# Performance work log

Hardware: AMD Instinct MI355X
Metric: run time of the kernel (lower is better)

Reference implementation:

```python
import jax, jax.numpy as jnp
import numpy as np

N, F, H = 4096, 256, 4

def setup_inputs() -> dict:
    key = jax.random.key(0)
    kx, kw, kb = jax.random.split(key, 3)
    x = jax.random.normal(kx, (N, F), dtype=jnp.float32)
    # per-head Linear(2F -> 1): weight [H, 2F], bias [H]
    lim = 1.0 / np.sqrt(2 * F)
    W = jax.random.uniform(kw, (H, 2 * F), minval=-lim, maxval=lim, dtype=jnp.float32)
    b = jax.random.uniform(kb, (H,), minval=-lim, maxval=lim, dtype=jnp.float32)
    return {"x": x, "W": W, "b": b}

def reference(x, W, b):
    n, f = x.shape
    # concat(x_i, x_j) @ w^T == x_i @ w1 + x_j @ w2  (separable score, same math)
    W1, W2 = W[:, :f], W[:, f:]            # [H,F] each
    s_i = x @ W1.T                          # [N,H] contribution of row node i
    s_j = x @ W2.T                          # [N,H] contribution of col node j
    # logits[h,i,j] = s_i[i,h] + s_j[j,h] + b[h]
    logits = s_i.T[:, :, None] + s_j.T[:, None, :] + b[:, None, None]  # [H,N,N]
    attn = jax.nn.softmax(logits, axis=2)   # softmax over neighbors j
    out_heads = jnp.einsum('hij,jf->hif', attn, x)  # [H,N,F]
    avg = jnp.mean(out_heads, axis=0)       # [N,F]
    return jax.nn.leaky_relu(avg, negative_slope=0.2)
```

## Files before the change

### kernel.cpp

```cpp
#include <hip/hip_runtime.h>


#define NROWS 4096
#define FDIM  256
#define HHEADS 4
#define RPB 64
#define NB1 (NROWS / RPB)
#define PAD 260


__global__ __launch_bounds__(256) void k1_partials(const float* __restrict__ x,
                                                   const float* __restrict__ W,
                                                   float* __restrict__ partU,
                                                   float* __restrict__ partZ) {
    __shared__ float x_lds[RPB * PAD];
    __shared__ float w_lds[HHEADS * FDIM];
    __shared__ float e_lds[RPB * HHEADS];

    const int t = threadIdx.x;
    const int row0 = blockIdx.x * RPB;

    for (int i = t; i < HHEADS * FDIM; i += 256) {
        int h = i >> 8, c = i & 255;
        w_lds[i] = W[h * (2 * FDIM) + FDIM + c];
    }
    for (int i = t; i < RPB * (FDIM / 4); i += 256) {
        int r = i >> 6, c4 = i & 63;
        float4 v = ((const float4*)x)[(size_t)(row0 + r) * (FDIM / 4) + c4];
        *(float4*)&x_lds[r * PAD + c4 * 4] = v;
    }
    __syncthreads();

    {
        int r = t >> 2, h = t & 3;
        const float4* xr = (const float4*)&x_lds[r * PAD];
        const float4* wr = (const float4*)&w_lds[h * FDIM];
        float acc = 0.f;
        #pragma unroll 8
        for (int c = 0; c < FDIM / 4; ++c) {
            float4 a = xr[c], b = wr[c];
            acc = fmaf(a.x, b.x, fmaf(a.y, b.y, fmaf(a.z, b.z, fmaf(a.w, b.w, acc))));
        }
        e_lds[r * 4 + h] = __expf(acc);
    }
    __syncthreads();

    if (t < HHEADS) {
        float z = 0.f;
        for (int r = 0; r < RPB; ++r) z += e_lds[r * 4 + t];
        partZ[blockIdx.x * HHEADS + t] = z;
    }

    float a0 = 0.f, a1 = 0.f, a2 = 0.f, a3 = 0.f;
    for (int r = 0; r < RPB; ++r) {
        float xv = x_lds[r * PAD + t];
        float4 e4 = *(const float4*)&e_lds[r * 4];
        a0 = fmaf(e4.x, xv, a0);
        a1 = fmaf(e4.y, xv, a1);
        a2 = fmaf(e4.z, xv, a2);
        a3 = fmaf(e4.w, xv, a3);
    }
    float* pu = partU + (size_t)blockIdx.x * (HHEADS * FDIM);
    pu[0 * FDIM + t] = a0;
    pu[1 * FDIM + t] = a1;
    pu[2 * FDIM + t] = a2;
    pu[3 * FDIM + t] = a3;
}

__global__ __launch_bounds__(256) void k2_out(const float* __restrict__ partU,
                                              const float* __restrict__ partZ,
                                              float* __restrict__ out) {
    __shared__ float v_lds[FDIM];
    __shared__ float zinv[HHEADS];
    const int t = threadIdx.x;

    if (t < HHEADS) {
        float z = 0.f;
        for (int b = 0; b < NB1; ++b) z += partZ[b * HHEADS + t];
        zinv[t] = 1.0f / z;
    }

    float u0 = 0.f, u1 = 0.f, u2 = 0.f, u3 = 0.f;
    for (int b = 0; b < NB1; ++b) {
        const float* p = partU + (size_t)b * (HHEADS * FDIM);
        u0 += p[0 * FDIM + t];
        u1 += p[1 * FDIM + t];
        u2 += p[2 * FDIM + t];
        u3 += p[3 * FDIM + t];
    }
    __syncthreads();

    float val = 0.25f * (u0 * zinv[0] + u1 * zinv[1] + u2 * zinv[2] + u3 * zinv[3]);
    v_lds[t] = val > 0.f ? val : 0.2f * val;
    __syncthreads();

    const int row0 = blockIdx.x * 64;
    float4* out4 = (float4*)out;
    #pragma unroll
    for (int i = 0; i < 16; ++i) {
        int idx = t + i * 256;
        int r = idx >> 6, c4 = idx & 63;
        out4[(size_t)(row0 + r) * (FDIM / 4) + c4] = *(const float4*)&v_lds[c4 * 4];
    }
}

extern "C" void kernel_launch(void* const* d_in, const int* in_sizes, int n_in,
                              void* d_out, int out_size, void* d_ws, size_t ws_size,
                              hipStream_t stream) {
    const float* x = (const float*)d_in[0];
    const float* W = (const float*)d_in[1];
    float* partU = (float*)d_ws;
    float* partZ = partU + (size_t)NB1 * HHEADS * FDIM;
    float* out = (float*)d_out;

    k1_partials<<<NB1, 256, 0, stream>>>(x, W, partU, partZ);
    k2_out<<<NROWS / 64, 256, 0, stream>>>(partU, partZ, out);
}
```

Baseline: 74.34 us.

## Split reduction into a separate parallel kernel and widen the partial-sum grid

The first kernel now processes 32 rows per block over 128 blocks, and each row/head dot product is split across two threads and combined with a shuffle. The old output kernel, where every block redundantly summed all partials serially, is replaced by a small reduction kernel spread over 16 blocks that writes the 256-element result vector once. A separate broadcast kernel then fills the output from that vector. This removes redundant reduction work and raises parallelism, at the cost of a third kernel launch.

```diff
diff --git a/kernel.cpp b/kernel.cpp
--- a/kernel.cpp
+++ b/kernel.cpp
@@ -3,10 +3,10 @@
 
 #define NROWS 4096
 #define FDIM  256
-#define HHEADS 4
-#define RPB 64
-#define NB1 (NROWS / RPB)
-#define PAD 260
+#define HH    4
+#define RPB   32
+#define NB1   128
+#define PAD   260
 
 
 __global__ __launch_bounds__(256) void k1_partials(const float* __restrict__ x,
@@ -14,13 +14,13 @@
                                                    float* __restrict__ partU,
                                                    float* __restrict__ partZ) {
     __shared__ float x_lds[RPB * PAD];
-    __shared__ float w_lds[HHEADS * FDIM];
-    __shared__ float e_lds[RPB * HHEADS];
+    __shared__ float w_lds[HH * FDIM];
+    __shared__ float e_lds[RPB * HH];
 
     const int t = threadIdx.x;
     const int row0 = blockIdx.x * RPB;
 
-    for (int i = t; i < HHEADS * FDIM; i += 256) {
+    for (int i = t; i < HH * FDIM; i += 256) {
         int h = i >> 8, c = i & 255;
         w_lds[i] = W[h * (2 * FDIM) + FDIM + c];
     }
@@ -32,23 +32,25 @@
     __syncthreads();
 
     {
-        int r = t >> 2, h = t & 3;
+        int pair = t >> 1, half = t & 1;
+        int r = pair >> 2, h = pair & 3;
         const float4* xr = (const float4*)&x_lds[r * PAD];
         const float4* wr = (const float4*)&w_lds[h * FDIM];
         float acc = 0.f;
-        #pragma unroll 8
-        for (int c = 0; c < FDIM / 4; ++c) {
+        #pragma unroll
+        for (int c = half * 32; c < half * 32 + 32; ++c) {
             float4 a = xr[c], b = wr[c];
             acc = fmaf(a.x, b.x, fmaf(a.y, b.y, fmaf(a.z, b.z, fmaf(a.w, b.w, acc))));
         }
-        e_lds[r * 4 + h] = __expf(acc);
+        acc += __shfl_xor(acc, 1);
+        if (half == 0) e_lds[r * 4 + h] = __expf(acc);
     }
     __syncthreads();
 
-    if (t < HHEADS) {
+    if (t < HH) {
         float z = 0.f;
         for (int r = 0; r < RPB; ++r) z += e_lds[r * 4 + t];
-        partZ[blockIdx.x * HHEADS + t] = z;
+        partZ[blockIdx.x * HH + t] = z;
     }
 
     float a0 = 0.f, a1 = 0.f, a2 = 0.f, a3 = 0.f;
@@ -60,47 +62,64 @@
         a2 = fmaf(e4.z, xv, a2);
         a3 = fmaf(e4.w, xv, a3);
     }
-    float* pu = partU + (size_t)blockIdx.x * (HHEADS * FDIM);
+    float* pu = partU + (size_t)blockIdx.x * (HH * FDIM);
     pu[0 * FDIM + t] = a0;
     pu[1 * FDIM + t] = a1;
     pu[2 * FDIM + t] = a2;
     pu[3 * FDIM + t] = a3;
 }
 
-__global__ __launch_bounds__(256) void k2_out(const float* __restrict__ partU,
-                                              const float* __restrict__ partZ,
-                                              float* __restrict__ out) {
-    __shared__ float v_lds[FDIM];
-    __shared__ float zinv[HHEADS];
+__global__ __launch_bounds__(256) void kred(const float* __restrict__ partU,
+                                            const float* __restrict__ partZ,
+                                            float* __restrict__ v) {
+    __shared__ float red[4][HH][16];
+    __shared__ float zinv[HH];
     const int t = threadIdx.x;
+    const int cl = t & 15, h = (t >> 4) & 3, bq = t >> 6;
+    const int g = blockIdx.x;
 
-    if (t < HHEADS) {
+    float s = 0.f;
+    const int b0 = bq * (NB1 / 4);
+    #pragma unroll 8
+    for (int b = b0; b < b0 + NB1 / 4; ++b)
+        s += partU[(size_t)b * (HH * FDIM) + h * FDIM + g * 16 + cl];
+    red[bq][h][cl] = s;
+
+    if (t < HH) {
         float z = 0.f;
-        for (int b = 0; b < NB1; ++b) z += partZ[b * HHEADS + t];
-        zinv[t] = 1.0f / z;
-    }
-
-    float u0 = 0.f, u1 = 0.f, u2 = 0.f, u3 = 0.f;
-    for (int b = 0; b < NB1; ++b) {
-        const float* p = partU + (size_t)b * (HHEADS * FDIM);
-        u0 += p[0 * FDIM + t];
-        u1 += p[1 * FDIM + t];
-        u2 += p[2 * FDIM + t];
-        u3 += p[3 * FDIM + t];
+        #pragma unroll 8
+        for (int b = 0; b < NB1; ++b) z += partZ[b * HH + t];
+        zinv[t] = 0.25f / z;
     }
     __syncthreads();
 
-    float val = 0.25f * (u0 * zinv[0] + u1 * zinv[1] + u2 * zinv[2] + u3 * zinv[3]);
-    v_lds[t] = val > 0.f ? val : 0.2f * val;
+    if (t < 16) {
+        float val = 0.f;
+        #pragma unroll
+        for (int h2 = 0; h2 < HH; ++h2) {
+            float uh = red[0][h2][t] + red[1][h2][t] + red[2][h2][t] + red[3][h2][t];
+            val = fmaf(uh, zinv[h2], val);
+        }
+        val = val > 0.f ? val : 0.2f * val;
+        v[g * 16 + t] = val;
+    }
+}
+
+__global__ __launch_bounds__(256) void kbcast(const float* __restrict__ v,
+                                              float* __restrict__ out) {
+    __shared__ float v_lds[FDIM];
+    const int t = threadIdx.x;
+    v_lds[t] = v[t];
     __syncthreads();
 
-    const int row0 = blockIdx.x * 64;
+    const int row0 = blockIdx.x * 16;
+    const int c4 = t & 63;
+    float4 val4 = *(const float4*)&v_lds[c4 * 4];
     float4* out4 = (float4*)out;
     #pragma unroll
-    for (int i = 0; i < 16; ++i) {
-        int idx = t + i * 256;
-        int r = idx >> 6, c4 = idx & 63;
-        out4[(size_t)(row0 + r) * (FDIM / 4) + c4] = *(const float4*)&v_lds[c4 * 4];
+    for (int i = 0; i < 4; ++i) {
+        int r = (t >> 6) + i * 4;
+        out4[(size_t)(row0 + r) * (FDIM / 4) + c4] = val4;
     }
 }
 
@@ -110,9 +129,11 @@
     const float* x = (const float*)d_in[0];
     const float* W = (const float*)d_in[1];
     float* partU = (float*)d_ws;
-    float* partZ = partU + (size_t)NB1 * HHEADS * FDIM;
+    float* partZ = partU + (size_t)NB1 * HH * FDIM;
+    float* v     = partZ + NB1 * HH;
     float* out = (float*)d_out;
 
     k1_partials<<<NB1, 256, 0, stream>>>(x, W, partU, partZ);
-    k2_out<<<NROWS / 64, 256, 0, stream>>>(partU, partZ, out);
+    kred<<<16, 256, 0, stream>>>(partU, partZ, v);
+    kbcast<<<NROWS / 16, 256, 0, stream>>>(v, out);
 }
```

Result: faster. 72.70 us (-2.2%).
